# Kernel tuning notes

Measured on AMD Instinct MI355X. Metric: run time of the kernel, lower is better.

Reference implementation:

```python
import jax, jax.numpy as jnp
import numpy as np

N = 50000      # nodes
E = 800000     # edges (avg degree 16)
F = 32         # n_features
FOUT = 32      # n_features_out
L = 2          # n_layers (Message+Update pairs)
LEN = 10.0     # length_scale


def _mlp(x, w1, b1, w2, b2):
    # embedding.MLP: Linear -> SiLU -> Linear
    return jax.nn.silu(x @ w1 + b1) @ w2 + b2


def _posenc(d):
    # sinusoidal PositionalEncoder(F, length=LEN): ranks 1..F/2
    ranks = jnp.arange(1, F // 2 + 1, dtype=d.dtype)
    a = d[:, None] * ranks * (jnp.pi / LEN)           # [E, F/2]
    return jnp.concatenate([jnp.sin(a), jnp.cos(a)], axis=-1)  # [E, F]


def _painn(s, v, edge_index, edge_dist, edge_dir,
           mp_w1, mp_b1, mp_w2, mp_b2, mw_w1, mw_b1, mw_w2, mw_b2,
           u_U, u_V, u_w1, u_b1, u_w2, u_b2,
           ro_w1, ro_b1, ro_w2, ro_b2, ro_V):
    src, dst = edge_index[0], edge_index[1]
    pe = _posenc(edge_dist)                            # [E, F]
    dirb = edge_dir[:, None, :]                        # [E, 1, 3]
    for l in range(L):
        # ---- Message ----
        mix = _mlp(s[src], mp_w1[l], mp_b1[l], mp_w2[l], mp_b2[l]) \
            * _mlp(pe, mw_w1[l], mw_b1[l], mw_w2[l], mw_b2[l])     # [E, 4F]
        gates, cpg, sed, sf = jnp.split(mix, 4, axis=-1)
        cross = jnp.cross(dirb, v[dst])                # [E, F, 3] (broadcast)
        dv = sed[:, :, None] * dirb + gates[:, :, None] * v[src] \
           + cpg[:, :, None] * cross                   # [E, F, 3]
        ds = sf * s[src]                               # [E, F]
        v = v + jax.ops.segment_sum(dv, dst, num_segments=N)
        s = s + jax.ops.segment_sum(ds, dst, num_segments=N)
        # ---- Update ----
        Vv = jnp.einsum('nfc,fg->ngc', v, u_V[l])      # [N, F, 3]
        Uv = jnp.einsum('nfc,fg->ngc', v, u_U[l])
        Vn = jnp.linalg.norm(Vv, axis=-1)              # [N, F]
        g, ssn, add = jnp.split(
            _mlp(jnp.concatenate([Vn, s], axis=-1), u_w1[l], u_b1[l], u_w2[l], u_b2[l]),
            3, axis=-1)
        v = v + g[:, :, None] * Uv
        s = s + Vn * Vn * ssn + add
    # ---- Readout ----
    inv_out, gates = jnp.split(_mlp(s, ro_w1, ro_b1, ro_w2, ro_b2), 2, axis=-1)
    eqv_out = gates[:, :, None] * jnp.einsum('nfc,fg->ngc', v, ro_V)
    return inv_out, eqv_out


def setup_inputs() -> dict:
    key = jax.random.key(0)
    ks = iter(jax.random.split(key, 64))
    nk = lambda: next(ks)
    lin = lambda fin, fout, *lead: (jax.random.normal(nk(), (*lead, fin, fout), jnp.float32)
                                    / np.sqrt(fin).astype(np.float32))
    d = {}
    d['invariant_node_features'] = jax.random.normal(nk(), (N, F), jnp.float32)
    d['equivariant_node_features'] = jax.random.normal(nk(), (N, F, 3), jnp.float32)
    d['edge_index'] = jax.random.randint(nk(), (2, E), 0, N)
    d['edge_dist'] = jax.random.uniform(nk(), (E,), jnp.float32) * LEN
    g = jax.random.normal(nk(), (E, 3), jnp.float32)
    d['edge_dir'] = g / jnp.linalg.norm(g, axis=-1, keepdims=True)
    # Message MLPs (phi on node features, W on positional encoding)
    d['mp_w1'] = lin(F, F, L); d['mp_b1'] = jnp.zeros((L, F), jnp.float32)
    d['mp_w2'] = lin(F, 4 * F, L); d['mp_b2'] = jnp.zeros((L, 4 * F), jnp.float32)
    d['mw_w1'] = lin(F, F, L); d['mw_b1'] = jnp.zeros((L, F), jnp.float32)
    d['mw_w2'] = lin(F, 4 * F, L); d['mw_b2'] = jnp.zeros((L, 4 * F), jnp.float32)
    # Update: EquivariantLinear U, V and MLP(2F -> F -> 3F)
    d['u_U'] = lin(F, F, L); d['u_V'] = lin(F, F, L)
    d['u_w1'] = lin(2 * F, F, L); d['u_b1'] = jnp.zeros((L, F), jnp.float32)
    d['u_w2'] = lin(F, 3 * F, L); d['u_b2'] = jnp.zeros((L, 3 * F), jnp.float32)
    # Readout: MLP(F -> F -> 2*FOUT) and EquivariantLinear V (F -> FOUT)
    d['ro_w1'] = lin(F, F); d['ro_b1'] = jnp.zeros((F,), jnp.float32)
    d['ro_w2'] = lin(F, 2 * FOUT); d['ro_b2'] = jnp.zeros((2 * FOUT,), jnp.float32)
    d['ro_V'] = lin(F, FOUT)
    return d


def reference(invariant_node_features, equivariant_node_features, edge_index,
              edge_dist, edge_dir,
              mp_w1, mp_b1, mp_w2, mp_b2, mw_w1, mw_b1, mw_w2, mw_b2,
              u_U, u_V, u_w1, u_b1, u_w2, u_b2,
              ro_w1, ro_b1, ro_w2, ro_b2, ro_V):
    return _painn(invariant_node_features, equivariant_node_features, edge_index,
                  edge_dist, edge_dir,
                  mp_w1, mp_b1, mp_w2, mp_b2, mw_w1, mw_b1, mw_w2, mw_b2,
                  u_U, u_V, u_w1, u_b1, u_w2, u_b2,
                  ro_w1, ro_b1, ro_w2, ro_b2, ro_V)
```

## Files before the change

### kernel.cpp

```cpp
#include <hip/hip_runtime.h>
#include <math.h>

#define PI_LEN 0.3141592653589793f
#define LEN_F  10.0f
#define TBL    4096

__device__ __forceinline__ float fsilu(float x) {
  return x * __builtin_amdgcn_rcpf(1.f + __expf(-x));
}

__global__ __launch_bounds__(256) void hist_kernel(const int* __restrict__ ei,
                                                   int* __restrict__ deg, int E_) {
  int e = blockIdx.x * 256 + threadIdx.x;
  if (e < E_) atomicAdd(&deg[ei[E_ + e]], 1);
}

__device__ __forceinline__ void tbl_role(
    int i, int g, int t,
    const float* __restrict__ w1, const float* __restrict__ b1,
    const float* __restrict__ w2, const float* __restrict__ b2,
    float4* __restrict__ tbl4, float (*pe)[32], float (*hl)[32])
{
  bool okt = (t <= TBL);
  float d = (float)t * (LEN_F / (float)TBL);
  pe[i][g] = (g < 16) ? __sinf(d * (float)(g + 1) * PI_LEN)
                      : __cosf(d * (float)(g - 15) * PI_LEN);
  float h = b1[g];
  for (int k = 0; k < 32; ++k) h += pe[i][k] * w1[k*32 + g];
  hl[i][g] = fsilu(h);
  float o0 = b2[g], o1 = b2[32+g], o2 = b2[64+g], o3 = b2[96+g];
  for (int k = 0; k < 32; ++k) {
    float hk = hl[i][k];
    o0 += hk * w2[k*128 +      g];
    o1 += hk * w2[k*128 + 32 + g];
    o2 += hk * w2[k*128 + 64 + g];
    o3 += hk * w2[k*128 + 96 + g];
  }
  if (okt) tbl4[(long)t*32 + g] = make_float4(o0, o1, o2, o3);
}

__global__ __launch_bounds__(1024) void scan_prep_kernel(
    const int* __restrict__ deg, int* __restrict__ off,
    int* __restrict__ cursor, int N_,
    const float* __restrict__ s,
    const float* __restrict__ mpw1, const float* __restrict__ mpb1,
    const float* __restrict__ mpw2, const float* __restrict__ mpb2,
    const float* __restrict__ mww1a, const float* __restrict__ mwb1a,
    const float* __restrict__ mww2a, const float* __restrict__ mwb2a,
    const float* __restrict__ mww1b, const float* __restrict__ mwb1b,
    const float* __restrict__ mww2b, const float* __restrict__ mwb2b,
    float4* __restrict__ Aout4a, float4* __restrict__ tbl4a,
    float4* __restrict__ tbl4b, int nodeB32, int tblB32)
{
  __shared__ float xs[32][32];
  __shared__ float hs[32][32];
  __shared__ int wtot[16];
  __shared__ int carry_s;
  int bid = blockIdx.x;
  int tid = threadIdx.x;
  if (bid == 0) {
    int lane = tid & 63, wid = tid >> 6;
    if (tid == 0) carry_s = 0;
// ... 129 lines not shown
    for (int b = 0; b < 4; ++b)
      EDGE_MATH(ed[b], m0[b], m1[b], fr[b], A[b], vs0[b], vs1[b], vs2[b]);
  }
  int p = pstart + nfull * 8 + hf;
  for (; p + 2 < pend; p += 4) {
    int  s0_ = srcp[p], s1_ = srcp[p + 2];
    float4 e0 = edata[p], e1 = edata[p + 2];
    float x0 = e0.w * inv_step, x1 = e1.w * inv_step;
    float f0 = floorf(x0), f1 = floorf(x1);
    int i0 = (int)f0; if (i0 > TBL - 1) i0 = TBL - 1;
    int i1 = (int)f1; if (i1 > TBL - 1) i1 = TBL - 1;
    float r0 = x0 - f0, r1 = x1 - f1;
    float4 a0 = tbl4[(long)i0*32 + g], b0 = tbl4[(long)(i0+1)*32 + g];
    float4 a1 = tbl4[(long)i1*32 + g], b1 = tbl4[(long)(i1+1)*32 + g];
    float4 A0 = Aout4[(long)s0_*32 + g], A1 = Aout4[(long)s1_*32 + g];
    const float* vq0 = v_prev + (long)s0_*96 + g*3;
    const float* vq1 = v_prev + (long)s1_*96 + g*3;
    float u0 = vq0[0], u1 = vq0[1], u2 = vq0[2];
    float t0 = vq1[0], t1 = vq1[1], t2 = vq1[2];
    EDGE_MATH(e0, a0, b0, r0, A0, u0, u1, u2);
    EDGE_MATH(e1, a1, b1, r1, A1, t0, t1, t2);
  }
  if (p < pend) {
    int  s0_ = srcp[p];
    float4 e0 = edata[p];
    float x0 = e0.w * inv_step;
    float f0 = floorf(x0);
    int i0 = (int)f0; if (i0 > TBL - 1) i0 = TBL - 1;
    float r0 = x0 - f0;
    float4 a0 = tbl4[(long)i0*32 + g], b0 = tbl4[(long)(i0+1)*32 + g];
    float4 A0 = Aout4[(long)s0_*32 + g];
    const float* vq0 = v_prev + (long)s0_*96 + g*3;
    float u0 = vq0[0], u1 = vq0[1], u2 = vq0[2];
    EDGE_MATH(e0, a0, b0, r0, A0, u0, u1, u2);
  }
  av0   += __shfl_xor(av0, 32);
  av1   += __shfl_xor(av1, 32);
  av2   += __shfl_xor(av2, 32);
  acc_s += __shfl_xor(acc_s, 32);
  if (hf == 0) acc4[(long)n*32 + g] = make_float4(av0, av1, av2, acc_s);
}

__global__ __launch_bounds__(256) void update_mid_kernel(
    const float* __restrict__ s_prev, const float* __restrict__ v_prev,
    const float4* __restrict__ acc4,
    const float* __restrict__ uU, const float* __restrict__ uV,
    const float* __restrict__ uw1, const float* __restrict__ ub1,
    const float* __restrict__ uw2, const float* __restrict__ ub2,
    const float* __restrict__ nw1, const float* __restrict__ nb1,
    const float* __restrict__ nw2, const float* __restrict__ nb2,
    float* __restrict__ s_out, float* __restrict__ v_out,
    float4* __restrict__ Aout4b, int N_)
{
  __shared__ float vld[4][96];
  __shared__ float in64[4][64];
  __shared__ float hld[4][32];
  int tid = threadIdx.x, w = tid >> 6, lane = tid & 63, g = lane & 31, hf = lane >> 5;
  long n = (long)blockIdx.x * 4 + w;
  if (n >= N_) return;
  float4 a = acc4[n*32 + g];
  const float* vp = v_prev + n*96 + g*3;
  float nv0 = vp[0] + a.x, nv1 = vp[1] + a.y, nv2 = vp[2] + a.z;
  float ns  = s_prev[n*32 + g] + a.w;
  if (hf == 0) { vld[w][g*3+0] = nv0; vld[w][g*3+1] = nv1; vld[w][g*3+2] = nv2; }
  float Vv0=0,Vv1=0,Vv2=0,Uv0=0,Uv1=0,Uv2=0;
  for (int j = 0; j < 16; ++j) {
    int f = hf * 16 + j;
    float wu = uU[f*32 + g];
    float wv = uV[f*32 + g];
    float v0 = vld[w][f*3+0], v1 = vld[w][f*3+1], v2 = vld[w][f*3+2];
    Vv0 += v0*wv; Vv1 += v1*wv; Vv2 += v2*wv;
    Uv0 += v0*wu; Uv1 += v1*wu; Uv2 += v2*wu;
  }
  Vv0 += __shfl_xor(Vv0, 32); Vv1 += __shfl_xor(Vv1, 32); Vv2 += __shfl_xor(Vv2, 32);
  Uv0 += __shfl_xor(Uv0, 32); Uv1 += __shfl_xor(Uv1, 32); Uv2 += __shfl_xor(Uv2, 32);
  float Vn = sqrtf(Vv0*Vv0 + Vv1*Vv1 + Vv2*Vv2);
  if (hf == 0) { in64[w][g] = Vn; in64[w][32 + g] = ns; }
  float h = 0.f;
  for (int j = 0; j < 32; ++j) {
    int k = hf * 32 + j;
    h += in64[w][k] * uw1[k*32 + g];
  }
  h += __shfl_xor(h, 32);
  h = fsilu(h + ub1[g]);
  if (hf == 0) hld[w][g] = h;
  float og = 0.f, ossn = 0.f, oadd = 0.f;
  for (int j = 0; j < 16; ++j) {
    int k = hf * 16 + j;
    float hk = hld[w][k];
    og   += hk * uw2[k*96 +      g];
    ossn += hk * uw2[k*96 + 32 + g];
    oadd += hk * uw2[k*96 + 64 + g];
  }
  og   += __shfl_xor(og, 32);
  ossn += __shfl_xor(ossn, 32);
  oadd += __shfl_xor(oadd, 32);
  og += ub2[g]; ossn += ub2[32 + g]; oadd += ub2[64 + g];
  float s_fin = ns + Vn*Vn*ossn + oadd;
  if (hf == 0) {
    float* vo = v_out + n*96 + g*3;
    vo[0] = nv0 + og*Uv0;
    vo[1] = nv1 + og*Uv1;
    vo[2] = nv2 + og*Uv2;
    s_out[n*32 + g] = s_fin;
  }
  if (hf == 0) in64[w][g] = s_fin;
  float h2 = 0.f;
  for (int j = 0; j < 16; ++j) {
    int k = hf * 16 + j;
    h2 += in64[w][k] * nw1[k*32 + g];
  }
  h2 += __shfl_xor(h2, 32);
  h2 = fsilu(h2 + nb1[g]);
  if (hf == 0) hld[w][g] = h2;
  float o0 = 0.f, o1 = 0.f, o2 = 0.f, o3 = 0.f;
  for (int j = 0; j < 16; ++j) {
    int k = hf * 16 + j;
    float hk = hld[w][k];
    o0 += hk * nw2[k*128 +      g];
    o1 += hk * nw2[k*128 + 32 + g];
    o2 += hk * nw2[k*128 + 64 + g];
    o3 += hk * nw2[k*128 + 96 + g];
  }
  o0 += __shfl_xor(o0, 32); o1 += __shfl_xor(o1, 32);
  o2 += __shfl_xor(o2, 32); o3 += __shfl_xor(o3, 32);
  o0 += nb2[g]; o1 += nb2[32+g]; o2 += nb2[64+g]; o3 += nb2[96+g];
  if (hf == 0) Aout4b[n*32 + g] = make_float4(o0, o1, o2, o3 * s_fin);
}

__global__ __launch_bounds__(256) void update_fin_kernel(
    const float* __restrict__ s_prev, const float* __restrict__ v_prev,
    const float4* __restrict__ acc4,
    const float* __restrict__ uU, const float* __restrict__ uV,
    const float* __restrict__ uw1, const float* __restrict__ ub1,
    const float* __restrict__ uw2, const float* __restrict__ ub2,
    const float* __restrict__ rw1, const float* __restrict__ rb1,
    const float* __restrict__ rw2, const float* __restrict__ rb2,
    const float* __restrict__ roV, float* __restrict__ out, int N_)
{
  __shared__ float vld[4][96];
  __shared__ float in64[4][64];
  __shared__ float hld[4][32];
  int tid = threadIdx.x, w = tid >> 6, lane = tid & 63, g = lane & 31, hf = lane >> 5;
  long n = (long)blockIdx.x * 4 + w;
  if (n >= N_) return;
  float4 a = acc4[n*32 + g];
  const float* vp = v_prev + n*96 + g*3;
  float nv0 = vp[0] + a.x, nv1 = vp[1] + a.y, nv2 = vp[2] + a.z;
  float ns  = s_prev[n*32 + g] + a.w;
  if (hf == 0) { vld[w][g*3+0] = nv0; vld[w][g*3+1] = nv1; vld[w][g*3+2] = nv2; }
  float Vv0=0,Vv1=0,Vv2=0,Uv0=0,Uv1=0,Uv2=0;
  for (int j = 0; j < 16; ++j) {
    int f = hf * 16 + j;
    float wu = uU[f*32 + g];
    float wv = uV[f*32 + g];
    float v0 = vld[w][f*3+0], v1 = vld[w][f*3+1], v2 = vld[w][f*3+2];
    Vv0 += v0*wv; Vv1 += v1*wv; Vv2 += v2*wv;
    Uv0 += v0*wu; Uv1 += v1*wu; Uv2 += v2*wu;
  }
  Vv0 += __shfl_xor(Vv0, 32); Vv1 += __shfl_xor(Vv1, 32); Vv2 += __shfl_xor(Vv2, 32);
  Uv0 += __shfl_xor(Uv0, 32); Uv1 += __shfl_xor(Uv1, 32); Uv2 += __shfl_xor(Uv2, 32);
  float Vn = sqrtf(Vv0*Vv0 + Vv1*Vv1 + Vv2*Vv2);
  if (hf == 0) { in64[w][g] = Vn; in64[w][32 + g] = ns; }
  float h = 0.f;
  for (int j = 0; j < 32; ++j) {
    int k = hf * 32 + j;
    h += in64[w][k] * uw1[k*32 + g];
  }
  h += __shfl_xor(h, 32);
  h = fsilu(h + ub1[g]);
  if (hf == 0) hld[w][g] = h;
  float og = 0.f, ossn = 0.f, oadd = 0.f;
  for (int j = 0; j < 16; ++j) {
    int k = hf * 16 + j;
    float hk = hld[w][k];
    og   += hk * uw2[k*96 +      g];
    ossn += hk * uw2[k*96 + 32 + g];
    oadd += hk * uw2[k*96 + 64 + g];
  }
  og   += __shfl_xor(og, 32);
  ossn += __shfl_xor(ossn, 32);
  oadd += __shfl_xor(oadd, 32);
  og += ub2[g]; ossn += ub2[32 + g]; oadd += ub2[64 + g];
  float s_fin = ns + Vn*Vn*ossn + oadd;
  float vf0 = nv0 + og*Uv0, vf1 = nv1 + og*Uv1, vf2 = nv2 + og*Uv2;
  if (hf == 0) in64[w][g] = s_fin;
  float h2 = 0.f;
  for (int j = 0; j < 16; ++j) {
    int k = hf * 16 + j;
    h2 += in64[w][k] * rw1[k*32 + g];
  }
  h2 += __shfl_xor(h2, 32);
  h2 = fsilu(h2 + rb1[g]);
  if (hf == 0) hld[w][g] = h2;
  float inv = 0.f, gate = 0.f;
  for (int j = 0; j < 16; ++j) {
    int k = hf * 16 + j;
    float hk = hld[w][k];
    inv  += hk * rw2[k*64 +      g];
    gate += hk * rw2[k*64 + 32 + g];
  }
  inv  += __shfl_xor(inv, 32);
  gate += __shfl_xor(gate, 32);
  inv += rb2[g]; gate += rb2[32 + g];
  if (hf == 0) { vld[w][g*3+0] = vf0; vld[w][g*3+1] = vf1; vld[w][g*3+2] = vf2; }
  float R0 = 0, R1 = 0, R2 = 0;
  for (int j = 0; j < 16; ++j) {
    int f = hf * 16 + j;
    float wv = roV[f*32 + g];
    R0 += vld[w][f*3+0]*wv; R1 += vld[w][f*3+1]*wv; R2 += vld[w][f*3+2]*wv;
  }
  R0 += __shfl_xor(R0, 32); R1 += __shfl_xor(R1, 32); R2 += __shfl_xor(R2, 32);
  if (hf == 0) {
    out[n*32 + g] = inv;
    long eb = (long)N_*32 + n*96 + (long)g*3;
    out[eb+0] = gate*R0; out[eb+1] = gate*R1; out[eb+2] = gate*R2;
  }
}

extern "C" void kernel_launch(void* const* d_in, const int* in_sizes, int n_in,
                              void* d_out, int out_size, void* d_ws, size_t ws_size,
                              hipStream_t stream)
{
  const float* s_in  = (const float*)d_in[0];
  const float* v_in  = (const float*)d_in[1];
  const int*   ei    = (const int*)  d_in[2];
  const float* dist  = (const float*)d_in[3];
  const float* edir  = (const float*)d_in[4];
  const float* mp_w1 = (const float*)d_in[5];
  const float* mp_b1 = (const float*)d_in[6];
  const float* mp_w2 = (const float*)d_in[7];
  const float* mp_b2 = (const float*)d_in[8];
  const float* mw_w1 = (const float*)d_in[9];
  const float* mw_b1 = (const float*)d_in[10];
  const float* mw_w2 = (const float*)d_in[11];
  const float* mw_b2 = (const float*)d_in[12];
  const float* u_U   = (const float*)d_in[13];
  const float* u_V   = (const float*)d_in[14];
  const float* u_w1  = (const float*)d_in[15];
  const float* u_b1  = (const float*)d_in[16];
  const float* u_w2  = (const float*)d_in[17];
  const float* u_b2  = (const float*)d_in[18];
  const float* ro_w1 = (const float*)d_in[19];
  const float* ro_b1 = (const float*)d_in[20];
  const float* ro_w2 = (const float*)d_in[21];
  const float* ro_b2 = (const float*)d_in[22];
  const float* ro_V  = (const float*)d_in[23];

  int N_ = in_sizes[0] / 32;
  int E_ = in_sizes[3];

  float*  sB    = (float*)d_ws;
  float*  vB    = sB + (size_t)N_*32;
  float4* Aout4a= (float4*)(vB + (size_t)N_*96);
  float4* Aout4b= Aout4a + (size_t)N_*32;
  float4* acc4b = Aout4b + (size_t)N_*32;
  float4* tbl4a = acc4b + (size_t)N_*32;
  float4* tbl4b = tbl4a + (size_t)(TBL+1)*32;
  float4* edata = tbl4b + (size_t)(TBL+1)*32;
  int*    srcp  = (int*)(edata + (size_t)E_);
  int*    deg   = srcp + E_;
  int*    off   = deg + N_;
  int*    cursor= off + N_ + 1;

  float4* acc4a = (float4*)d_out;

  int gathBlocks = (N_ + 3) / 4;
  int updBlocks  = (N_ + 3) / 4;
  int edgeBlocks = (E_ + 255) / 256;
  int nodeB32    = (N_ + 31) / 32;
  int tblB32     = (TBL + 1 + 31) / 32;

  hipMemsetAsync(deg, 0, (size_t)N_ * sizeof(int), stream);
  hist_kernel<<<edgeBlocks, 256, 0, stream>>>(ei, deg, E_);

  scan_prep_kernel<<<1 + nodeB32 + 2*tblB32, 1024, 0, stream>>>(
      deg, off, cursor, N_, s_in,
      mp_w1, mp_b1, mp_w2, mp_b2,
      mw_w1, mw_b1, mw_w2, mw_b2,
      mw_w1 + 1024, mw_b1 + 32, mw_w2 + 4096, mw_b2 + 128,
      Aout4a, tbl4a, tbl4b, nodeB32, tblB32);

  scatter_kernel<<<edgeBlocks, 256, 0, stream>>>(ei, dist, edir, cursor, srcp, edata, E_);

  gather_kernel<<<gathBlocks, 256, 0, stream>>>(
      off, srcp, edata, tbl4a, v_in, Aout4a, acc4a, N_);
  update_mid_kernel<<<updBlocks, 256, 0, stream>>>(
      s_in, v_in, acc4a,
      u_U, u_V, u_w1, u_b1, u_w2, u_b2,
      mp_w1 + 1024, mp_b1 + 32, mp_w2 + 4096, mp_b2 + 128,
      sB, vB, Aout4b, N_);

  gather_kernel<<<gathBlocks, 256, 0, stream>>>(
      off, srcp, edata, tbl4b, vB, Aout4b, acc4b, N_);
  update_fin_kernel<<<updBlocks, 256, 0, stream>>>(
      sB, vB, acc4b,
      u_U + 1024, u_V + 1024, u_w1 + 2048, u_b1 + 32, u_w2 + 3072, u_b2 + 96,
      ro_w1, ro_b1, ro_w2, ro_b2, ro_V, (float*)d_out, N_);
}
```

Before: 611.3 us.

## Tile update kernels over 32 nodes per block with register-blocked node dot products

Rewrites both update kernels so that each 256-thread block handles 32 nodes instead of 4. Each thread computes one output feature for 4 nodes, reading padded, transposed shared-memory tiles as float4. Each weight value is loaded once per 4 nodes rather than once per node, and the half-wave shuffle reductions are gone. The cost is more registers, more shared memory, and extra block-wide barriers between stages.

```diff
diff --git a/kernel.cpp b/kernel.cpp
--- a/kernel.cpp
+++ b/kernel.cpp
@@ -4,10 +4,13 @@
 #define PI_LEN 0.3141592653589793f
 #define LEN_F  10.0f
 #define TBL    4096
+#define UPAD   36
 
 __device__ __forceinline__ float fsilu(float x) {
   return x * __builtin_amdgcn_rcpf(1.f + __expf(-x));
 }
+
+#define F4Q(v, q) (((const float*)&(v))[q])
 
 __global__ __launch_bounds__(256) void hist_kernel(const int* __restrict__ ei,
                                                    int* __restrict__ deg, int E_) {
@@ -243,80 +246,132 @@
     float* __restrict__ s_out, float* __restrict__ v_out,
     float4* __restrict__ Aout4b, int N_)
 {
-  __shared__ float vld[4][96];
-  __shared__ float in64[4][64];
-  __shared__ float hld[4][32];
-  int tid = threadIdx.x, w = tid >> 6, lane = tid & 63, g = lane & 31, hf = lane >> 5;
-  long n = (long)blockIdx.x * 4 + w;
-  if (n >= N_) return;
-  float4 a = acc4[n*32 + g];
-  const float* vp = v_prev + n*96 + g*3;
-  float nv0 = vp[0] + a.x, nv1 = vp[1] + a.y, nv2 = vp[2] + a.z;
-  float ns  = s_prev[n*32 + g] + a.w;
-  if (hf == 0) { vld[w][g*3+0] = nv0; vld[w][g*3+1] = nv1; vld[w][g*3+2] = nv2; }
-  float Vv0=0,Vv1=0,Vv2=0,Uv0=0,Uv1=0,Uv2=0;
-  for (int j = 0; j < 16; ++j) {
-    int f = hf * 16 + j;
-    float wu = uU[f*32 + g];
-    float wv = uV[f*32 + g];
-    float v0 = vld[w][f*3+0], v1 = vld[w][f*3+1], v2 = vld[w][f*3+2];
-    Vv0 += v0*wv; Vv1 += v1*wv; Vv2 += v2*wv;
-    Uv0 += v0*wu; Uv1 += v1*wu; Uv2 += v2*wu;
-  }
-  Vv0 += __shfl_xor(Vv0, 32); Vv1 += __shfl_xor(Vv1, 32); Vv2 += __shfl_xor(Vv2, 32);
-  Uv0 += __shfl_xor(Uv0, 32); Uv1 += __shfl_xor(Uv1, 32); Uv2 += __shfl_xor(Uv2, 32);
-  float Vn = sqrtf(Vv0*Vv0 + Vv1*Vv1 + Vv2*Vv2);
-  if (hf == 0) { in64[w][g] = Vn; in64[w][32 + g] = ns; }
-  float h = 0.f;
-  for (int j = 0; j < 32; ++j) {
-    int k = hf * 32 + j;
-    h += in64[w][k] * uw1[k*32 + g];
-  }
-  h += __shfl_xor(h, 32);
-  h = fsilu(h + ub1[g]);
-  if (hf == 0) hld[w][g] = h;
-  float og = 0.f, ossn = 0.f, oadd = 0.f;
-  for (int j = 0; j < 16; ++j) {
-    int k = hf * 16 + j;
-    float hk = hld[w][k];
-    og   += hk * uw2[k*96 +      g];
-    ossn += hk * uw2[k*96 + 32 + g];
-    oadd += hk * uw2[k*96 + 64 + g];
-  }
-  og   += __shfl_xor(og, 32);
-  ossn += __shfl_xor(ossn, 32);
-  oadd += __shfl_xor(oadd, 32);
-  og += ub2[g]; ossn += ub2[32 + g]; oadd += ub2[64 + g];
-  float s_fin = ns + Vn*Vn*ossn + oadd;
-  if (hf == 0) {
-    float* vo = v_out + n*96 + g*3;
-    vo[0] = nv0 + og*Uv0;
-    vo[1] = nv1 + og*Uv1;
-    vo[2] = nv2 + og*Uv2;
-    s_out[n*32 + g] = s_fin;
-  }
-  if (hf == 0) in64[w][g] = s_fin;
-  float h2 = 0.f;
-  for (int j = 0; j < 16; ++j) {
-    int k = hf * 16 + j;
-    h2 += in64[w][k] * nw1[k*32 + g];
-  }
-  h2 += __shfl_xor(h2, 32);
-  h2 = fsilu(h2 + nb1[g]);
-  if (hf == 0) hld[w][g] = h2;
-  float o0 = 0.f, o1 = 0.f, o2 = 0.f, o3 = 0.f;
-  for (int j = 0; j < 16; ++j) {
-    int k = hf * 16 + j;
-    float hk = hld[w][k];
-    o0 += hk * nw2[k*128 +      g];
-    o1 += hk * nw2[k*128 + 32 + g];
-    o2 += hk * nw2[k*128 + 64 + g];
-    o3 += hk * nw2[k*128 + 96 + g];
-  }
-  o0 += __shfl_xor(o0, 32); o1 += __shfl_xor(o1, 32);
-  o2 += __shfl_xor(o2, 32); o3 += __shfl_xor(o3, 32);
-  o0 += nb2[g]; o1 += nb2[32+g]; o2 += nb2[64+g]; o3 += nb2[96+g];
-  if (hf == 0) Aout4b[n*32 + g] = make_float4(o0, o1, o2, o3 * s_fin);
+  __shared__ float aV[3][32][UPAD];
+  __shared__ float aS[32][UPAD];
+  __shared__ float aN[32][UPAD];
+  __shared__ float aH[32][UPAD];
+  int tid = threadIdx.x, g = tid & 31, i = tid >> 5;
+  int base = blockIdx.x * 32;
+  int mb = i * 4;
+  #pragma unroll
+  for (int p = 0; p < 4; ++p) {
+    int m = i + p * 8;
+    long n = base + m;
+    float4 a = make_float4(0.f, 0.f, 0.f, 0.f);
+    float v0 = 0, v1 = 0, v2 = 0, sv = 0;
+    if (n < N_) {
+      a = acc4[n*32 + g];
+      const float* vp = v_prev + n*96 + g*3;
+      v0 = vp[0]; v1 = vp[1]; v2 = vp[2];
+      sv = s_prev[n*32 + g];
+    }
+    aV[0][g][m] = v0 + a.x;
+    aV[1][g][m] = v1 + a.y;
+    aV[2][g][m] = v2 + a.z;
+    aS[g][m]    = sv + a.w;
+  }
+  __syncthreads();
+  float Vv0[4] = {}, Vv1[4] = {}, Vv2[4] = {};
+  float Uv0[4] = {}, Uv1[4] = {}, Uv2[4] = {};
+  for (int k = 0; k < 32; ++k) {
+    float wv = uV[k*32 + g];
+    float wu = uU[k*32 + g];
+    float4 a0 = *(const float4*)&aV[0][k][mb];
+    float4 a1 = *(const float4*)&aV[1][k][mb];
+    float4 a2 = *(const float4*)&aV[2][k][mb];
+    #pragma unroll
+    for (int q = 0; q < 4; ++q) {
+      float x0 = F4Q(a0, q), x1 = F4Q(a1, q), x2 = F4Q(a2, q);
+      Vv0[q] += x0*wv; Vv1[q] += x1*wv; Vv2[q] += x2*wv;
+      Uv0[q] += x0*wu; Uv1[q] += x1*wu; Uv2[q] += x2*wu;
+    }
+  }
+  float Vn[4];
+  #pragma unroll
+  for (int q = 0; q < 4; ++q) {
+    Vn[q] = sqrtf(Vv0[q]*Vv0[q] + Vv1[q]*Vv1[q] + Vv2[q]*Vv2[q]);
+    aN[g][mb + q] = Vn[q];
+  }
+  __syncthreads();
+  float h[4] = {};
+  for (int k = 0; k < 32; ++k) {
+    float w1a = uw1[k*32 + g];
+    float w1b = uw1[(32 + k)*32 + g];
+    float4 vn = *(const float4*)&aN[k][mb];
+    float4 sq = *(const float4*)&aS[k][mb];
+    #pragma unroll
+    for (int q = 0; q < 4; ++q) h[q] += F4Q(vn, q)*w1a + F4Q(sq, q)*w1b;
+  }
+  float bb1 = ub1[g];
+  #pragma unroll
+  for (int q = 0; q < 4; ++q) { h[q] = fsilu(h[q] + bb1); aH[g][mb + q] = h[q]; }
+  __syncthreads();
+  float og[4] = {}, ossn[4] = {}, oadd[4] = {};
+  for (int k = 0; k < 32; ++k) {
+    float wg_ = uw2[k*96 +      g];
+    float ws_ = uw2[k*96 + 32 + g];
+    float wa_ = uw2[k*96 + 64 + g];
+    float4 hq = *(const float4*)&aH[k][mb];
+    #pragma unroll
+    for (int q = 0; q < 4; ++q) {
+      float hv = F4Q(hq, q);
+      og[q] += hv*wg_; ossn[q] += hv*ws_; oadd[q] += hv*wa_;
+    }
+  }
+  float b2g = ub2[g], b2s = ub2[32 + g], b2a = ub2[64 + g];
+  float4 nsq = *(const float4*)&aS[g][mb];
+  float sfin[4];
+  #pragma unroll
+  for (int q = 0; q < 4; ++q) {
+    og[q] += b2g;
+    sfin[q] = F4Q(nsq, q) + Vn[q]*Vn[q]*(ossn[q] + b2s) + (oadd[q] + b2a);
+    long n = base + mb + q;
+    if (n < N_) {
+      float* vo = v_out + n*96 + g*3;
+      vo[0] = aV[0][g][mb + q] + og[q]*Uv0[q];
+      vo[1] = aV[1][g][mb + q] + og[q]*Uv1[q];
+      vo[2] = aV[2][g][mb + q] + og[q]*Uv2[q];
+      s_out[n*32 + g] = sfin[q];
+    }
+  }
+  #pragma unroll
+  for (int q = 0; q < 4; ++q) aN[g][mb + q] = sfin[q];
+  __syncthreads();
+  float h2[4] = {};
+  for (int k = 0; k < 32; ++k) {
+    float w = nw1[k*32 + g];
+    float4 xq = *(const float4*)&aN[k][mb];
+    #pragma unroll
+    for (int q = 0; q < 4; ++q) h2[q] += F4Q(xq, q)*w;
+  }
+  float nb1g = nb1[g];
+  #pragma unroll
+  for (int q = 0; q < 4; ++q) { h2[q] = fsilu(h2[q] + nb1g); }
+  __syncthreads();
+  #pragma unroll
+  for (int q = 0; q < 4; ++q) aH[g][mb + q] = h2[q];
+  __syncthreads();
+  float o0[4] = {}, o1[4] = {}, o2[4] = {}, o3[4] = {};
+  for (int k = 0; k < 32; ++k) {
+    float w0 = nw2[k*128 +      g];
+    float w1 = nw2[k*128 + 32 + g];
+    float w2_ = nw2[k*128 + 64 + g];
+    float w3 = nw2[k*128 + 96 + g];
+    float4 hq = *(const float4*)&aH[k][mb];
+    #pragma unroll
+    for (int q = 0; q < 4; ++q) {
+      float hv = F4Q(hq, q);
+      o0[q] += hv*w0; o1[q] += hv*w1; o2[q] += hv*w2_; o3[q] += hv*w3;
+    }
+  }
+  float c0 = nb2[g], c1 = nb2[32+g], c2 = nb2[64+g], c3 = nb2[96+g];
+  #pragma unroll
+  for (int q = 0; q < 4; ++q) {
+    long n = base + mb + q;
+    if (n < N_)
+      Aout4b[n*32 + g] = make_float4(o0[q] + c0, o1[q] + c1, o2[q] + c2,
+                                     (o3[q] + c3) * sfin[q]);
+  }
 }
 
 __global__ __launch_bounds__(256) void update_fin_kernel(
@@ -329,83 +384,144 @@
     const float* __restrict__ rw2, const float* __restrict__ rb2,
     const float* __restrict__ roV, float* __restrict__ out, int N_)
 {
-  __shared__ float vld[4][96];
-  __shared__ float in64[4][64];
-  __shared__ float hld[4][32];
-  int tid = threadIdx.x, w = tid >> 6, lane = tid & 63, g = lane & 31, hf = lane >> 5;
-  long n = (long)blockIdx.x * 4 + w;
-  if (n >= N_) return;
-  float4 a = acc4[n*32 + g];
-  const float* vp = v_prev + n*96 + g*3;
-  float nv0 = vp[0] + a.x, nv1 = vp[1] + a.y, nv2 = vp[2] + a.z;
-  float ns  = s_prev[n*32 + g] + a.w;
-  if (hf == 0) { vld[w][g*3+0] = nv0; vld[w][g*3+1] = nv1; vld[w][g*3+2] = nv2; }
-  float Vv0=0,Vv1=0,Vv2=0,Uv0=0,Uv1=0,Uv2=0;
-  for (int j = 0; j < 16; ++j) {
-    int f = hf * 16 + j;
-    float wu = uU[f*32 + g];
-    float wv = uV[f*32 + g];
-    float v0 = vld[w][f*3+0], v1 = vld[w][f*3+1], v2 = vld[w][f*3+2];
-    Vv0 += v0*wv; Vv1 += v1*wv; Vv2 += v2*wv;
-    Uv0 += v0*wu; Uv1 += v1*wu; Uv2 += v2*wu;
-  }
-  Vv0 += __shfl_xor(Vv0, 32); Vv1 += __shfl_xor(Vv1, 32); Vv2 += __shfl_xor(Vv2, 32);
-  Uv0 += __shfl_xor(Uv0, 32); Uv1 += __shfl_xor(Uv1, 32); Uv2 += __shfl_xor(Uv2, 32);
-  float Vn = sqrtf(Vv0*Vv0 + Vv1*Vv1 + Vv2*Vv2);
-  if (hf == 0) { in64[w][g] = Vn; in64[w][32 + g] = ns; }
-  float h = 0.f;
-  for (int j = 0; j < 32; ++j) {
-    int k = hf * 32 + j;
-    h += in64[w][k] * uw1[k*32 + g];
-  }
-  h += __shfl_xor(h, 32);
-  h = fsilu(h + ub1[g]);
-  if (hf == 0) hld[w][g] = h;
-  float og = 0.f, ossn = 0.f, oadd = 0.f;
-  for (int j = 0; j < 16; ++j) {
-    int k = hf * 16 + j;
-    float hk = hld[w][k];
-    og   += hk * uw2[k*96 +      g];
-    ossn += hk * uw2[k*96 + 32 + g];
-    oadd += hk * uw2[k*96 + 64 + g];
-  }
-  og   += __shfl_xor(og, 32);
-  ossn += __shfl_xor(ossn, 32);
-  oadd += __shfl_xor(oadd, 32);
-  og += ub2[g]; ossn += ub2[32 + g]; oadd += ub2[64 + g];
-  float s_fin = ns + Vn*Vn*ossn + oadd;
-  float vf0 = nv0 + og*Uv0, vf1 = nv1 + og*Uv1, vf2 = nv2 + og*Uv2;
-  if (hf == 0) in64[w][g] = s_fin;
-  float h2 = 0.f;
-  for (int j = 0; j < 16; ++j) {
-    int k = hf * 16 + j;
-    h2 += in64[w][k] * rw1[k*32 + g];
-  }
-  h2 += __shfl_xor(h2, 32);
-  h2 = fsilu(h2 + rb1[g]);
-  if (hf == 0) hld[w][g] = h2;
-  float inv = 0.f, gate = 0.f;
-  for (int j = 0; j < 16; ++j) {
-    int k = hf * 16 + j;
-    float hk = hld[w][k];
-    inv  += hk * rw2[k*64 +      g];
-    gate += hk * rw2[k*64 + 32 + g];
-  }
-  inv  += __shfl_xor(inv, 32);
-  gate += __shfl_xor(gate, 32);
-  inv += rb2[g]; gate += rb2[32 + g];
-  if (hf == 0) { vld[w][g*3+0] = vf0; vld[w][g*3+1] = vf1; vld[w][g*3+2] = vf2; }
-  float R0 = 0, R1 = 0, R2 = 0;
-  for (int j = 0; j < 16; ++j) {
-    int f = hf * 16 + j;
-    float wv = roV[f*32 + g];
-    R0 += vld[w][f*3+0]*wv; R1 += vld[w][f*3+1]*wv; R2 += vld[w][f*3+2]*wv;
-  }
-  R0 += __shfl_xor(R0, 32); R1 += __shfl_xor(R1, 32); R2 += __shfl_xor(R2, 32);
-  if (hf == 0) {
-    out[n*32 + g] = inv;
-    long eb = (long)N_*32 + n*96 + (long)g*3;
-    out[eb+0] = gate*R0; out[eb+1] = gate*R1; out[eb+2] = gate*R2;
+  __shared__ float aV[3][32][UPAD];
+  __shared__ float aS[32][UPAD];
+  __shared__ float aN[32][UPAD];
+  __shared__ float aH[32][UPAD];
+  int tid = threadIdx.x, g = tid & 31, i = tid >> 5;
+  int base = blockIdx.x * 32;
+  int mb = i * 4;
+  #pragma unroll
+  for (int p = 0; p < 4; ++p) {
+    int m = i + p * 8;
+    long n = base + m;
+    float4 a = make_float4(0.f, 0.f, 0.f, 0.f);
+    float v0 = 0, v1 = 0, v2 = 0, sv = 0;
+    if (n < N_) {
+      a = acc4[n*32 + g];
+      const float* vp = v_prev + n*96 + g*3;
+      v0 = vp[0]; v1 = vp[1]; v2 = vp[2];
+      sv = s_prev[n*32 + g];
+    }
+    aV[0][g][m] = v0 + a.x;
+    aV[1][g][m] = v1 + a.y;
+    aV[2][g][m] = v2 + a.z;
+    aS[g][m]    = sv + a.w;
+  }
+  __syncthreads();
+  float Vv0[4] = {}, Vv1[4] = {}, Vv2[4] = {};
+  float Uv0[4] = {}, Uv1[4] = {}, Uv2[4] = {};
+  for (int k = 0; k < 32; ++k) {
+    float wv = uV[k*32 + g];
+    float wu = uU[k*32 + g];
+    float4 a0 = *(const float4*)&aV[0][k][mb];
+    float4 a1 = *(const float4*)&aV[1][k][mb];
+    float4 a2 = *(const float4*)&aV[2][k][mb];
+    #pragma unroll
+    for (int q = 0; q < 4; ++q) {
+      float x0 = F4Q(a0, q), x1 = F4Q(a1, q), x2 = F4Q(a2, q);
+      Vv0[q] += x0*wv; Vv1[q] += x1*wv; Vv2[q] += x2*wv;
+      Uv0[q] += x0*wu; Uv1[q] += x1*wu; Uv2[q] += x2*wu;
+    }
+  }
+  float Vn[4];
+  #pragma unroll
+  for (int q = 0; q < 4; ++q) {
+    Vn[q] = sqrtf(Vv0[q]*Vv0[q] + Vv1[q]*Vv1[q] + Vv2[q]*Vv2[q]);
+    aN[g][mb + q] = Vn[q];
+  }
+  __syncthreads();
+  float h[4] = {};
+  for (int k = 0; k < 32; ++k) {
+    float w1a = uw1[k*32 + g];
+    float w1b = uw1[(32 + k)*32 + g];
+    float4 vn = *(const float4*)&aN[k][mb];
+    float4 sq = *(const float4*)&aS[k][mb];
+    #pragma unroll
+    for (int q = 0; q < 4; ++q) h[q] += F4Q(vn, q)*w1a + F4Q(sq, q)*w1b;
+  }
+  float bb1 = ub1[g];
+  #pragma unroll
+  for (int q = 0; q < 4; ++q) { h[q] = fsilu(h[q] + bb1); aH[g][mb + q] = h[q]; }
+  __syncthreads();
+  float og[4] = {}, ossn[4] = {}, oadd[4] = {};
+  for (int k = 0; k < 32; ++k) {
+    float wg_ = uw2[k*96 +      g];
+    float ws_ = uw2[k*96 + 32 + g];
+    float wa_ = uw2[k*96 + 64 + g];
+    float4 hq = *(const float4*)&aH[k][mb];
+    #pragma unroll
+    for (int q = 0; q < 4; ++q) {
+      float hv = F4Q(hq, q);
+      og[q] += hv*wg_; ossn[q] += hv*ws_; oadd[q] += hv*wa_;
+    }
+  }
+  float b2g = ub2[g], b2s = ub2[32 + g], b2a = ub2[64 + g];
+  float4 nsq = *(const float4*)&aS[g][mb];
+  float sfin[4], vf0[4], vf1[4], vf2[4];
+  #pragma unroll
+  for (int q = 0; q < 4; ++q) {
+    og[q] += b2g;
+    sfin[q] = F4Q(nsq, q) + Vn[q]*Vn[q]*(ossn[q] + b2s) + (oadd[q] + b2a);
+    vf0[q] = aV[0][g][mb + q] + og[q]*Uv0[q];
+    vf1[q] = aV[1][g][mb + q] + og[q]*Uv1[q];
+    vf2[q] = aV[2][g][mb + q] + og[q]*Uv2[q];
+  }
+  __syncthreads();
+  #pragma unroll
+  for (int q = 0; q < 4; ++q) {
+    aN[g][mb + q] = sfin[q];
+    aV[0][g][mb + q] = vf0[q];
+    aV[1][g][mb + q] = vf1[q];
+    aV[2][g][mb + q] = vf2[q];
+  }
+  __syncthreads();
+  float h2[4] = {};
+  for (int k = 0; k < 32; ++k) {
+    float w = rw1[k*32 + g];
+    float4 xq = *(const float4*)&aN[k][mb];
+    #pragma unroll
+    for (int q = 0; q < 4; ++q) h2[q] += F4Q(xq, q)*w;
+  }
+  float rb1g = rb1[g];
+  #pragma unroll
+  for (int q = 0; q < 4; ++q) h2[q] = fsilu(h2[q] + rb1g);
+  __syncthreads();
+  #pragma unroll
+  for (int q = 0; q < 4; ++q) aH[g][mb + q] = h2[q];
+  __syncthreads();
+  float inv[4] = {}, gate[4] = {};
+  for (int k = 0; k < 32; ++k) {
+    float w0 = rw2[k*64 +      g];
+    float w1 = rw2[k*64 + 32 + g];
+    float4 hq = *(const float4*)&aH[k][mb];
+    #pragma unroll
+    for (int q = 0; q < 4; ++q) {
+      float hv = F4Q(hq, q);
+      inv[q] += hv*w0; gate[q] += hv*w1;
+    }
+  }
+  float R0[4] = {}, R1[4] = {}, R2[4] = {};
+  for (int k = 0; k < 32; ++k) {
+    float w = roV[k*32 + g];
+    float4 a0 = *(const float4*)&aV[0][k][mb];
+    float4 a1 = *(const float4*)&aV[1][k][mb];
+    float4 a2 = *(const float4*)&aV[2][k][mb];
+    #pragma unroll
+    for (int q = 0; q < 4; ++q) {
+      R0[q] += F4Q(a0, q)*w; R1[q] += F4Q(a1, q)*w; R2[q] += F4Q(a2, q)*w;
+    }
+  }
+  float rb2g = rb2[g], rb2h = rb2[32 + g];
+  #pragma unroll
+  for (int q = 0; q < 4; ++q) {
+    long n = base + mb + q;
+    if (n < N_) {
+      out[n*32 + g] = inv[q] + rb2g;
+      float gt = gate[q] + rb2h;
+      long eb = (long)N_*32 + n*96 + (long)g*3;
+      out[eb+0] = gt*R0[q]; out[eb+1] = gt*R1[q]; out[eb+2] = gt*R2[q];
+    }
   }
 }
 
@@ -457,7 +573,7 @@
   float4* acc4a = (float4*)d_out;
 
   int gathBlocks = (N_ + 3) / 4;
-  int updBlocks  = (N_ + 3) / 4;
+  int updBlocks  = (N_ + 31) / 32;
   int edgeBlocks = (E_ + 255) / 256;
   int nodeB32    = (N_ + 31) / 32;
   int tblB32     = (TBL + 1 + 31) / 32;
```

Result: slower. 696.9 us (+14.0%).

## Process two nodes per wavefront in update kernels to share weight loads

Applied to the files above, without the earlier changes.

The update_mid and update_fin kernels now assign two nodes to each 64-lane wavefront, one per half-wave, instead of one. Each half still computes a split-K partial product for both nodes, so every weight load from global or cache is reused across two nodes and all 64 lanes write useful output. The launch grid is halved. The cost is more registers and shared memory per block, which could lower occupancy.

```diff
diff --git a/kernel.cpp b/kernel.cpp
--- a/kernel.cpp
+++ b/kernel.cpp
@@ -243,80 +243,107 @@
     float* __restrict__ s_out, float* __restrict__ v_out,
     float4* __restrict__ Aout4b, int N_)
 {
-  __shared__ float vld[4][96];
-  __shared__ float in64[4][64];
-  __shared__ float hld[4][32];
+  __shared__ float vA_[4][96], vB_[4][96];
+  __shared__ float inA[4][64], inB[4][64];
+  __shared__ float hA_[4][32], hB_[4][32];
   int tid = threadIdx.x, w = tid >> 6, lane = tid & 63, g = lane & 31, hf = lane >> 5;
-  long n = (long)blockIdx.x * 4 + w;
-  if (n >= N_) return;
-  float4 a = acc4[n*32 + g];
-  const float* vp = v_prev + n*96 + g*3;
-  float nv0 = vp[0] + a.x, nv1 = vp[1] + a.y, nv2 = vp[2] + a.z;
-  float ns  = s_prev[n*32 + g] + a.w;
-  if (hf == 0) { vld[w][g*3+0] = nv0; vld[w][g*3+1] = nv1; vld[w][g*3+2] = nv2; }
-  float Vv0=0,Vv1=0,Vv2=0,Uv0=0,Uv1=0,Uv2=0;
-  for (int j = 0; j < 16; ++j) {
-    int f = hf * 16 + j;
-    float wu = uU[f*32 + g];
-    float wv = uV[f*32 + g];
-    float v0 = vld[w][f*3+0], v1 = vld[w][f*3+1], v2 = vld[w][f*3+2];
-    Vv0 += v0*wv; Vv1 += v1*wv; Vv2 += v2*wv;
-    Uv0 += v0*wu; Uv1 += v1*wu; Uv2 += v2*wu;
-  }
-  Vv0 += __shfl_xor(Vv0, 32); Vv1 += __shfl_xor(Vv1, 32); Vv2 += __shfl_xor(Vv2, 32);
-  Uv0 += __shfl_xor(Uv0, 32); Uv1 += __shfl_xor(Uv1, 32); Uv2 += __shfl_xor(Uv2, 32);
-  float Vn = sqrtf(Vv0*Vv0 + Vv1*Vv1 + Vv2*Vv2);
-  if (hf == 0) { in64[w][g] = Vn; in64[w][32 + g] = ns; }
-  float h = 0.f;
+  long nown = (long)blockIdx.x * 8 + 2*w + hf;
+  bool ok = (nown < N_);
+  float nv0 = 0, nv1 = 0, nv2 = 0, ns = 0;
+  if (ok) {
+    float4 a = acc4[nown*32 + g];
+    const float* vp = v_prev + nown*96 + g*3;
+    nv0 = vp[0] + a.x; nv1 = vp[1] + a.y; nv2 = vp[2] + a.z;
+    ns  = s_prev[nown*32 + g] + a.w;
+  }
+  if (hf == 0) {
+    vA_[w][g*3+0] = nv0; vA_[w][g*3+1] = nv1; vA_[w][g*3+2] = nv2;
+    inA[w][32+g] = ns;
+  } else {
+    vB_[w][g*3+0] = nv0; vB_[w][g*3+1] = nv1; vB_[w][g*3+2] = nv2;
+    inB[w][32+g] = ns;
+  }
+  float VvA0=0,VvA1=0,VvA2=0,UvA0=0,UvA1=0,UvA2=0;
+  float VvB0=0,VvB1=0,VvB2=0,UvB0=0,UvB1=0,UvB2=0;
+  for (int j = 0; j < 16; ++j) {
+    int k = hf*16 + j;
+    float wv = uV[k*32 + g], wu = uU[k*32 + g];
+    float a0 = vA_[w][k*3+0], a1 = vA_[w][k*3+1], a2 = vA_[w][k*3+2];
+    float b0 = vB_[w][k*3+0], b1 = vB_[w][k*3+1], b2 = vB_[w][k*3+2];
+    VvA0 += a0*wv; VvA1 += a1*wv; VvA2 += a2*wv;
+    UvA0 += a0*wu; UvA1 += a1*wu; UvA2 += a2*wu;
+    VvB0 += b0*wv; VvB1 += b1*wv; VvB2 += b2*wv;
+    UvB0 += b0*wu; UvB1 += b1*wu; UvB2 += b2*wu;
+  }
+  VvA0 += __shfl_xor(VvA0,32); VvA1 += __shfl_xor(VvA1,32); VvA2 += __shfl_xor(VvA2,32);
+  UvA0 += __shfl_xor(UvA0,32); UvA1 += __shfl_xor(UvA1,32); UvA2 += __shfl_xor(UvA2,32);
+  VvB0 += __shfl_xor(VvB0,32); VvB1 += __shfl_xor(VvB1,32); VvB2 += __shfl_xor(VvB2,32);
+  UvB0 += __shfl_xor(UvB0,32); UvB1 += __shfl_xor(UvB1,32); UvB2 += __shfl_xor(UvB2,32);
+  float VnA = sqrtf(VvA0*VvA0 + VvA1*VvA1 + VvA2*VvA2);
+  float VnB = sqrtf(VvB0*VvB0 + VvB1*VvB1 + VvB2*VvB2);
+  float Vno = hf ? VnB : VnA;
+  float Uv0 = hf ? UvB0 : UvA0, Uv1 = hf ? UvB1 : UvA1, Uv2 = hf ? UvB2 : UvA2;
+  if (hf == 0) inA[w][g] = VnA; else inB[w][g] = VnB;
+  float hAa = 0, hBb = 0;
   for (int j = 0; j < 32; ++j) {
-    int k = hf * 32 + j;
-    h += in64[w][k] * uw1[k*32 + g];
-  }
-  h += __shfl_xor(h, 32);
-  h = fsilu(h + ub1[g]);
-  if (hf == 0) hld[w][g] = h;
-  float og = 0.f, ossn = 0.f, oadd = 0.f;
-  for (int j = 0; j < 16; ++j) {
-    int k = hf * 16 + j;
-    float hk = hld[w][k];
-    og   += hk * uw2[k*96 +      g];
-    ossn += hk * uw2[k*96 + 32 + g];
-    oadd += hk * uw2[k*96 + 64 + g];
-  }
-  og   += __shfl_xor(og, 32);
-  ossn += __shfl_xor(ossn, 32);
-  oadd += __shfl_xor(oadd, 32);
-  og += ub2[g]; ossn += ub2[32 + g]; oadd += ub2[64 + g];
-  float s_fin = ns + Vn*Vn*ossn + oadd;
-  if (hf == 0) {
-    float* vo = v_out + n*96 + g*3;
-    vo[0] = nv0 + og*Uv0;
-    vo[1] = nv1 + og*Uv1;
-    vo[2] = nv2 + og*Uv2;
-    s_out[n*32 + g] = s_fin;
-  }
-  if (hf == 0) in64[w][g] = s_fin;
-  float h2 = 0.f;
-  for (int j = 0; j < 16; ++j) {
-    int k = hf * 16 + j;
-    h2 += in64[w][k] * nw1[k*32 + g];
-  }
-  h2 += __shfl_xor(h2, 32);
-  h2 = fsilu(h2 + nb1[g]);
-  if (hf == 0) hld[w][g] = h2;
-  float o0 = 0.f, o1 = 0.f, o2 = 0.f, o3 = 0.f;
-  for (int j = 0; j < 16; ++j) {
-    int k = hf * 16 + j;
-    float hk = hld[w][k];
-    o0 += hk * nw2[k*128 +      g];
-    o1 += hk * nw2[k*128 + 32 + g];
-    o2 += hk * nw2[k*128 + 64 + g];
-    o3 += hk * nw2[k*128 + 96 + g];
-  }
-  o0 += __shfl_xor(o0, 32); o1 += __shfl_xor(o1, 32);
-  o2 += __shfl_xor(o2, 32); o3 += __shfl_xor(o3, 32);
-  o0 += nb2[g]; o1 += nb2[32+g]; o2 += nb2[64+g]; o3 += nb2[96+g];
-  if (hf == 0) Aout4b[n*32 + g] = make_float4(o0, o1, o2, o3 * s_fin);
+    int k = hf*32 + j;
+    float wk = uw1[k*32 + g];
+    hAa += inA[w][k]*wk; hBb += inB[w][k]*wk;
+  }
+  hAa += __shfl_xor(hAa, 32); hBb += __shfl_xor(hBb, 32);
+  float bb1 = ub1[g];
+  hAa = fsilu(hAa + bb1); hBb = fsilu(hBb + bb1);
+  if (hf == 0) hA_[w][g] = hAa; else hB_[w][g] = hBb;
+  float ogA=0, osA=0, oaA=0, ogB=0, osB=0, oaB=0;
+  for (int j = 0; j < 16; ++j) {
+    int k = hf*16 + j;
+    float w0 = uw2[k*96 + g], w1 = uw2[k*96 + 32 + g], w2 = uw2[k*96 + 64 + g];
+    float ha = hA_[w][k], hb = hB_[w][k];
+    ogA += ha*w0; osA += ha*w1; oaA += ha*w2;
+    ogB += hb*w0; osB += hb*w1; oaB += hb*w2;
+  }
+  ogA += __shfl_xor(ogA,32); osA += __shfl_xor(osA,32); oaA += __shfl_xor(oaA,32);
+  ogB += __shfl_xor(ogB,32); osB += __shfl_xor(osB,32); oaB += __shfl_xor(oaB,32);
+  float og_o = (hf ? ogB : ogA) + ub2[g];
+  float os_o = (hf ? osB : osA) + ub2[32 + g];
+  float oa_o = (hf ? oaB : oaA) + ub2[64 + g];
+  float sfin = ns + Vno*Vno*os_o + oa_o;
+  if (ok) {
+    float* vo = v_out + nown*96 + g*3;
+    vo[0] = nv0 + og_o*Uv0;
+    vo[1] = nv1 + og_o*Uv1;
+    vo[2] = nv2 + og_o*Uv2;
+    s_out[nown*32 + g] = sfin;
+  }
+  if (hf == 0) inA[w][g] = sfin; else inB[w][g] = sfin;
+  float h2A = 0, h2B = 0;
+  for (int j = 0; j < 16; ++j) {
+    int k = hf*16 + j;
+    float wk = nw1[k*32 + g];
+    h2A += inA[w][k]*wk; h2B += inB[w][k]*wk;
+  }
+  h2A += __shfl_xor(h2A, 32); h2B += __shfl_xor(h2B, 32);
+  float nb1g = nb1[g];
+  h2A = fsilu(h2A + nb1g); h2B = fsilu(h2B + nb1g);
+  if (hf == 0) hA_[w][g] = h2A; else hB_[w][g] = h2B;
+  float o0A=0,o1A=0,o2A=0,o3A=0, o0B=0,o1B=0,o2B=0,o3B=0;
+  for (int j = 0; j < 16; ++j) {
+    int k = hf*16 + j;
+    float w0 = nw2[k*128 + g],      w1 = nw2[k*128 + 32 + g];
+    float w2 = nw2[k*128 + 64 + g], w3 = nw2[k*128 + 96 + g];
+    float ha = hA_[w][k], hb = hB_[w][k];
+    o0A += ha*w0; o1A += ha*w1; o2A += ha*w2; o3A += ha*w3;
+    o0B += hb*w0; o1B += hb*w1; o2B += hb*w2; o3B += hb*w3;
+  }
+  o0A += __shfl_xor(o0A,32); o1A += __shfl_xor(o1A,32);
+  o2A += __shfl_xor(o2A,32); o3A += __shfl_xor(o3A,32);
+  o0B += __shfl_xor(o0B,32); o1B += __shfl_xor(o1B,32);
+  o2B += __shfl_xor(o2B,32); o3B += __shfl_xor(o3B,32);
+  float o0o = (hf ? o0B : o0A) + nb2[g];
+  float o1o = (hf ? o1B : o1A) + nb2[32 + g];
+  float o2o = (hf ? o2B : o2A) + nb2[64 + g];
+  float o3o = (hf ? o3B : o3A) + nb2[96 + g];
+  if (ok) Aout4b[nown*32 + g] = make_float4(o0o, o1o, o2o, o3o * sfin);
 }
 
 __global__ __launch_bounds__(256) void update_fin_kernel(
@@ -329,83 +356,115 @@
     const float* __restrict__ rw2, const float* __restrict__ rb2,
     const float* __restrict__ roV, float* __restrict__ out, int N_)
 {
-  __shared__ float vld[4][96];
-  __shared__ float in64[4][64];
-  __shared__ float hld[4][32];
+  __shared__ float vA_[4][96], vB_[4][96];
+  __shared__ float inA[4][64], inB[4][64];
+  __shared__ float hA_[4][32], hB_[4][32];
   int tid = threadIdx.x, w = tid >> 6, lane = tid & 63, g = lane & 31, hf = lane >> 5;
-  long n = (long)blockIdx.x * 4 + w;
-  if (n >= N_) return;
-  float4 a = acc4[n*32 + g];
-  const float* vp = v_prev + n*96 + g*3;
-  float nv0 = vp[0] + a.x, nv1 = vp[1] + a.y, nv2 = vp[2] + a.z;
-  float ns  = s_prev[n*32 + g] + a.w;
-  if (hf == 0) { vld[w][g*3+0] = nv0; vld[w][g*3+1] = nv1; vld[w][g*3+2] = nv2; }
-  float Vv0=0,Vv1=0,Vv2=0,Uv0=0,Uv1=0,Uv2=0;
-  for (int j = 0; j < 16; ++j) {
-    int f = hf * 16 + j;
-    float wu = uU[f*32 + g];
-    float wv = uV[f*32 + g];
-    float v0 = vld[w][f*3+0], v1 = vld[w][f*3+1], v2 = vld[w][f*3+2];
-    Vv0 += v0*wv; Vv1 += v1*wv; Vv2 += v2*wv;
-    Uv0 += v0*wu; Uv1 += v1*wu; Uv2 += v2*wu;
-  }
-  Vv0 += __shfl_xor(Vv0, 32); Vv1 += __shfl_xor(Vv1, 32); Vv2 += __shfl_xor(Vv2, 32);
-  Uv0 += __shfl_xor(Uv0, 32); Uv1 += __shfl_xor(Uv1, 32); Uv2 += __shfl_xor(Uv2, 32);
-  float Vn = sqrtf(Vv0*Vv0 + Vv1*Vv1 + Vv2*Vv2);
-  if (hf == 0) { in64[w][g] = Vn; in64[w][32 + g] = ns; }
-  float h = 0.f;
+  long nown = (long)blockIdx.x * 8 + 2*w + hf;
+  bool ok = (nown < N_);
+  float nv0 = 0, nv1 = 0, nv2 = 0, ns = 0;
+  if (ok) {
+    float4 a = acc4[nown*32 + g];
+    const float* vp = v_prev + nown*96 + g*3;
+    nv0 = vp[0] + a.x; nv1 = vp[1] + a.y; nv2 = vp[2] + a.z;
+    ns  = s_prev[nown*32 + g] + a.w;
+  }
+  if (hf == 0) {
+    vA_[w][g*3+0] = nv0; vA_[w][g*3+1] = nv1; vA_[w][g*3+2] = nv2;
+    inA[w][32+g] = ns;
+  } else {
+    vB_[w][g*3+0] = nv0; vB_[w][g*3+1] = nv1; vB_[w][g*3+2] = nv2;
+    inB[w][32+g] = ns;
+  }
+  float VvA0=0,VvA1=0,VvA2=0,UvA0=0,UvA1=0,UvA2=0;
+  float VvB0=0,VvB1=0,VvB2=0,UvB0=0,UvB1=0,UvB2=0;
+  for (int j = 0; j < 16; ++j) {
+    int k = hf*16 + j;
+    float wv = uV[k*32 + g], wu = uU[k*32 + g];
+    float a0 = vA_[w][k*3+0], a1 = vA_[w][k*3+1], a2 = vA_[w][k*3+2];
+    float b0 = vB_[w][k*3+0], b1 = vB_[w][k*3+1], b2 = vB_[w][k*3+2];
+    VvA0 += a0*wv; VvA1 += a1*wv; VvA2 += a2*wv;
+    UvA0 += a0*wu; UvA1 += a1*wu; UvA2 += a2*wu;
+    VvB0 += b0*wv; VvB1 += b1*wv; VvB2 += b2*wv;
+    UvB0 += b0*wu; UvB1 += b1*wu; UvB2 += b2*wu;
+  }
+  VvA0 += __shfl_xor(VvA0,32); VvA1 += __shfl_xor(VvA1,32); VvA2 += __shfl_xor(VvA2,32);
+  UvA0 += __shfl_xor(UvA0,32); UvA1 += __shfl_xor(UvA1,32); UvA2 += __shfl_xor(UvA2,32);
+  VvB0 += __shfl_xor(VvB0,32); VvB1 += __shfl_xor(VvB1,32); VvB2 += __shfl_xor(VvB2,32);
+  UvB0 += __shfl_xor(UvB0,32); UvB1 += __shfl_xor(UvB1,32); UvB2 += __shfl_xor(UvB2,32);
+  float VnA = sqrtf(VvA0*VvA0 + VvA1*VvA1 + VvA2*VvA2);
+  float VnB = sqrtf(VvB0*VvB0 + VvB1*VvB1 + VvB2*VvB2);
+  float Vno = hf ? VnB : VnA;
+  float Uv0 = hf ? UvB0 : UvA0, Uv1 = hf ? UvB1 : UvA1, Uv2 = hf ? UvB2 : UvA2;
+  if (hf == 0) inA[w][g] = VnA; else inB[w][g] = VnB;
+  float hAa = 0, hBb = 0;
   for (int j = 0; j < 32; ++j) {
-    int k = hf * 32 + j;
-    h += in64[w][k] * uw1[k*32 + g];
-  }
-  h += __shfl_xor(h, 32);
-  h = fsilu(h + ub1[g]);
-  if (hf == 0) hld[w][g] = h;
-  float og = 0.f, ossn = 0.f, oadd = 0.f;
-  for (int j = 0; j < 16; ++j) {
-    int k = hf * 16 + j;
-    float hk = hld[w][k];
-    og   += hk * uw2[k*96 +      g];
-    ossn += hk * uw2[k*96 + 32 + g];
-    oadd += hk * uw2[k*96 + 64 + g];
-  }
-  og   += __shfl_xor(og, 32);
-  ossn += __shfl_xor(ossn, 32);
-  oadd += __shfl_xor(oadd, 32);
-  og += ub2[g]; ossn += ub2[32 + g]; oadd += ub2[64 + g];
-  float s_fin = ns + Vn*Vn*ossn + oadd;
-  float vf0 = nv0 + og*Uv0, vf1 = nv1 + og*Uv1, vf2 = nv2 + og*Uv2;
-  if (hf == 0) in64[w][g] = s_fin;
-  float h2 = 0.f;
-  for (int j = 0; j < 16; ++j) {
-    int k = hf * 16 + j;
-    h2 += in64[w][k] * rw1[k*32 + g];
-  }
-  h2 += __shfl_xor(h2, 32);
-  h2 = fsilu(h2 + rb1[g]);
-  if (hf == 0) hld[w][g] = h2;
-  float inv = 0.f, gate = 0.f;
-  for (int j = 0; j < 16; ++j) {
-    int k = hf * 16 + j;
-    float hk = hld[w][k];
-    inv  += hk * rw2[k*64 +      g];
-    gate += hk * rw2[k*64 + 32 + g];
-  }
-  inv  += __shfl_xor(inv, 32);
-  gate += __shfl_xor(gate, 32);
-  inv += rb2[g]; gate += rb2[32 + g];
-  if (hf == 0) { vld[w][g*3+0] = vf0; vld[w][g*3+1] = vf1; vld[w][g*3+2] = vf2; }
-  float R0 = 0, R1 = 0, R2 = 0;
-  for (int j = 0; j < 16; ++j) {
-    int f = hf * 16 + j;
-    float wv = roV[f*32 + g];
-    R0 += vld[w][f*3+0]*wv; R1 += vld[w][f*3+1]*wv; R2 += vld[w][f*3+2]*wv;
-  }
-  R0 += __shfl_xor(R0, 32); R1 += __shfl_xor(R1, 32); R2 += __shfl_xor(R2, 32);
+    int k = hf*32 + j;
+    float wk = uw1[k*32 + g];
+    hAa += inA[w][k]*wk; hBb += inB[w][k]*wk;
+  }
+  hAa += __shfl_xor(hAa, 32); hBb += __shfl_xor(hBb, 32);
+  float bb1 = ub1[g];
+  hAa = fsilu(hAa + bb1); hBb = fsilu(hBb + bb1);
+  if (hf == 0) hA_[w][g] = hAa; else hB_[w][g] = hBb;
+  float ogA=0, osA=0, oaA=0, ogB=0, osB=0, oaB=0;
+  for (int j = 0; j < 16; ++j) {
+    int k = hf*16 + j;
+    float w0 = uw2[k*96 + g], w1 = uw2[k*96 + 32 + g], w2 = uw2[k*96 + 64 + g];
+    float ha = hA_[w][k], hb = hB_[w][k];
+    ogA += ha*w0; osA += ha*w1; oaA += ha*w2;
+    ogB += hb*w0; osB += hb*w1; oaB += hb*w2;
+  }
+  ogA += __shfl_xor(ogA,32); osA += __shfl_xor(osA,32); oaA += __shfl_xor(oaA,32);
+  ogB += __shfl_xor(ogB,32); osB += __shfl_xor(osB,32); oaB += __shfl_xor(oaB,32);
+  float og_o = (hf ? ogB : ogA) + ub2[g];
+  float os_o = (hf ? osB : osA) + ub2[32 + g];
+  float oa_o = (hf ? oaB : oaA) + ub2[64 + g];
+  float sfin = ns + Vno*Vno*os_o + oa_o;
+  float vf0 = nv0 + og_o*Uv0, vf1 = nv1 + og_o*Uv1, vf2 = nv2 + og_o*Uv2;
   if (hf == 0) {
-    out[n*32 + g] = inv;
-    long eb = (long)N_*32 + n*96 + (long)g*3;
-    out[eb+0] = gate*R0; out[eb+1] = gate*R1; out[eb+2] = gate*R2;
+    vA_[w][g*3+0] = vf0; vA_[w][g*3+1] = vf1; vA_[w][g*3+2] = vf2;
+    inA[w][g] = sfin;
+  } else {
+    vB_[w][g*3+0] = vf0; vB_[w][g*3+1] = vf1; vB_[w][g*3+2] = vf2;
+    inB[w][g] = sfin;
+  }
+  float h2A = 0, h2B = 0;
+  for (int j = 0; j < 16; ++j) {
+    int k = hf*16 + j;
+    float wk = rw1[k*32 + g];
+    h2A += inA[w][k]*wk; h2B += inB[w][k]*wk;
+  }
+  h2A += __shfl_xor(h2A, 32); h2B += __shfl_xor(h2B, 32);
+  float rb1g = rb1[g];
+  h2A = fsilu(h2A + rb1g); h2B = fsilu(h2B + rb1g);
+  if (hf == 0) hA_[w][g] = h2A; else hB_[w][g] = h2B;
+  float invA=0, gateA=0, invB=0, gateB=0;
+  for (int j = 0; j < 16; ++j) {
+    int k = hf*16 + j;
+    float w0 = rw2[k*64 + g], w1 = rw2[k*64 + 32 + g];
+    float ha = hA_[w][k], hb = hB_[w][k];
+    invA += ha*w0; gateA += ha*w1;
+    invB += hb*w0; gateB += hb*w1;
+  }
+  float R0A=0,R1A=0,R2A=0, R0B=0,R1B=0,R2B=0;
+  for (int j = 0; j < 16; ++j) {
+    int k = hf*16 + j;
+    float wk = roV[k*32 + g];
+    R0A += vA_[w][k*3+0]*wk; R1A += vA_[w][k*3+1]*wk; R2A += vA_[w][k*3+2]*wk;
+    R0B += vB_[w][k*3+0]*wk; R1B += vB_[w][k*3+1]*wk; R2B += vB_[w][k*3+2]*wk;
+  }
+  invA += __shfl_xor(invA,32); gateA += __shfl_xor(gateA,32);
+  invB += __shfl_xor(invB,32); gateB += __shfl_xor(gateB,32);
+  R0A += __shfl_xor(R0A,32); R1A += __shfl_xor(R1A,32); R2A += __shfl_xor(R2A,32);
+  R0B += __shfl_xor(R0B,32); R1B += __shfl_xor(R1B,32); R2B += __shfl_xor(R2B,32);
+  float inv_o  = (hf ? invB  : invA)  + rb2[g];
+  float gate_o = (hf ? gateB : gateA) + rb2[32 + g];
+  float R0o = hf ? R0B : R0A, R1o = hf ? R1B : R1A, R2o = hf ? R2B : R2A;
+  if (ok) {
+    out[nown*32 + g] = inv_o;
+    long eb = (long)N_*32 + nown*96 + (long)g*3;
+    out[eb+0] = gate_o*R0o; out[eb+1] = gate_o*R1o; out[eb+2] = gate_o*R2o;
   }
 }
 
@@ -457,7 +516,7 @@
   float4* acc4a = (float4*)d_out;
 
   int gathBlocks = (N_ + 3) / 4;
-  int updBlocks  = (N_ + 3) / 4;
+  int updBlocks  = (N_ + 7) / 8;
   int edgeBlocks = (E_ + 255) / 256;
   int nodeB32    = (N_ + 31) / 32;
   int tblB32     = (TBL + 1 + 31) / 32;
```

New measurement: 554.2 us (median of 2 runs). -9.3%, faster.
